# Performance work log

Measured on AMD Instinct MI355X. Metric: run time of the kernel, lower is better.

The kernel has to match this reference:

```python
import jax, jax.numpy as jnp
import numpy as np


def setup_inputs() -> dict:
    key = jax.random.key(0)
    ks = jax.random.split(key, 5)
    b, n, d = 1, 768, 128
    scale = 1.0 / np.sqrt(d)
    x = jax.random.normal(ks[0], (b, n, d), dtype=jnp.float32)
    W_in = jax.random.normal(ks[1], (d, d), dtype=jnp.float32) * scale
    b_in = jax.random.normal(ks[2], (d,), dtype=jnp.float32) * 0.02
    W_out = jax.random.normal(ks[3], (d, d), dtype=jnp.float32) * scale
    b_out = jax.random.normal(ks[4], (d,), dtype=jnp.float32) * 0.02
    return {"x": x, "W_in": W_in, "b_in": b_in, "W_out": W_out, "b_out": b_out}


def reference(x, W_in, b_in, W_out, b_out):
    # proj_in applied to x (original calls it twice on the same input; identical result)
    left = jnp.einsum('bid,ed->bie', x, W_in) + b_in          # [b, n, d]
    # broadcast outer product: [b, i, 1, d] * [b, 1, j, d] -> [b, i, j, d]
    outer = left[:, :, None, :] * left[:, None, :, :]
    # proj_out over feature dim
    out = jnp.einsum('bijd,ed->bije', outer, W_out) + b_out    # [b, n, n, d]
    return out
```

## Files before the change

### kernel.cpp

```cpp
#include <hip/hip_runtime.h>

#define Nn 768
#define Dd 128
#define LDP 136

typedef __attribute__((ext_vector_type(8))) short bf16x8;
typedef __attribute__((ext_vector_type(4))) float f32x4;
typedef __attribute__((ext_vector_type(4))) int   i32x4;

static __device__ __forceinline__ unsigned short f2bf(float f) {
  unsigned int u = __builtin_bit_cast(unsigned int, f);
  u += 0x7fffu + ((u >> 16) & 1u);
  return (unsigned short)(u >> 16);
}
static __device__ __forceinline__ float bf2f(unsigned short h) {
  unsigned int u = ((unsigned int)h) << 16;
  return __builtin_bit_cast(float, u);
}
static __device__ __forceinline__ unsigned int cvtpk(float lo, float hi) {
  unsigned int r;
  asm("v_cvt_pk_bf16_f32 %0, %1, %2" : "=v"(r) : "v"(lo), "v"(hi));
  return r;
}

__global__ __launch_bounds__(128)
void k_left(const float* __restrict__ x, const float* __restrict__ Win,
            const float* __restrict__ bin, unsigned short* __restrict__ left) {
  __shared__ float sx[Dd];
  const int i = blockIdx.x;
  const int e = threadIdx.x;
  sx[e] = x[i * Dd + e];
  __syncthreads();
  const float4* wrow = (const float4*)(Win + e * Dd);
  float a0 = 0.f, a1 = 0.f, a2 = 0.f, a3 = 0.f;
#pragma unroll
  for (int d4 = 0; d4 < Dd / 4; d4 += 4) {
    float4 w0 = wrow[d4+0], w1 = wrow[d4+1], w2 = wrow[d4+2], w3 = wrow[d4+3];
    a0 += sx[4*d4+ 0]*w0.x + sx[4*d4+ 1]*w0.y + sx[4*d4+ 2]*w0.z + sx[4*d4+ 3]*w0.w;
    a1 += sx[4*d4+ 4]*w1.x + sx[4*d4+ 5]*w1.y + sx[4*d4+ 6]*w1.z + sx[4*d4+ 7]*w1.w;
    a2 += sx[4*d4+ 8]*w2.x + sx[4*d4+ 9]*w2.y + sx[4*d4+10]*w2.z + sx[4*d4+11]*w2.w;
    a3 += sx[4*d4+12]*w3.x + sx[4*d4+13]*w3.y + sx[4*d4+14]*w3.z + sx[4*d4+15]*w3.w;
  }
  left[i * Dd + e] = f2bf(((a0 + a1) + (a2 + a3)) + bin[e]);
}

__global__ __launch_bounds__(256, 4)
void k_outer(const unsigned short* __restrict__ left, const float* __restrict__ Wout,
             const float* __restrict__ bout, float* __restrict__ out) {
  __shared__ __attribute__((aligned(16))) unsigned short sB[128 * LDP];
  __shared__ float sLi[Dd];
  __shared__ float sBo[Dd];

  const int jt = blockIdx.x;
  const int i  = blockIdx.y;
  const int t  = threadIdx.x;

  if (t < Dd) {
    sLi[t] = bf2f(left[i * Dd + t]);
    sBo[t] = bout[t];
  }
  __syncthreads();

  {
    const int row = t >> 4;
    const int c8  = (t & 15) * 8;
    float l[8];
#pragma unroll
    for (int q = 0; q < 8; ++q) l[q] = sLi[c8 + q];
#pragma unroll
    for (int it = 0; it < 8; ++it) {
      const int r = row + it * 16;
      const float4* wp = (const float4*)(Wout + r * Dd + c8);
      float4 w0 = wp[0], w1 = wp[1];
      i32x4 vb;
      vb[0] = (int)cvtpk(w0.x * l[0], w0.y * l[1]);
      vb[1] = (int)cvtpk(w0.z * l[2], w0.w * l[3]);
      vb[2] = (int)cvtpk(w1.x * l[4], w1.y * l[5]);
      vb[3] = (int)cvtpk(w1.z * l[6], w1.w * l[7]);
      *(i32x4*)(sB + r * LDP + c8) = vb;
    }
  }
  __syncthreads();

  const int wid  = t >> 6;
  const int lane = t & 63;
  const int l15  = lane & 15;
  const int kq   = (lane >> 4) * 8;

  float bias[8];
#pragma unroll
  for (int n = 0; n < 8; ++n) bias[n] = sBo[n * 16 + l15];

  const unsigned short* gA = left + (size_t)(jt * 128 + wid * 32 + l15) * Dd;
  bf16x8 A0[4], A1[4];
#pragma unroll
  for (int kb = 0; kb < 4; ++kb) {
    A0[kb] = *(const bf16x8*)(gA + kb * 32 + kq);
    A1[kb] = *(const bf16x8*)(gA + 16 * Dd + kb * 32 + kq);
  }

  f32x4 acc[2][8] = {};
#pragma unroll
  for (int n = 0; n < 8; ++n) {
    const unsigned short* sBrow = sB + (n * 16 + l15) * LDP + kq;
#pragma unroll
    for (int kb = 0; kb < 4; ++kb) {
      bf16x8 b = *(const bf16x8*)(sBrow + kb * 32);
      acc[0][n] = __builtin_amdgcn_mfma_f32_16x16x32_bf16(A0[kb], b, acc[0][n], 0, 0, 0);
      acc[1][n] = __builtin_amdgcn_mfma_f32_16x16x32_bf16(A1[kb], b, acc[1][n], 0, 0, 0);
    }
  }

#pragma unroll
  for (int jb = 0; jb < 2; ++jb) {
#pragma unroll
    for (int r = 0; r < 4; ++r) {
      const int j = jt * 128 + wid * 32 + jb * 16 + (lane >> 4) * 4 + r;
      float* orow = out + ((size_t)i * Nn + j) * Dd;
#pragma unroll
      for (int n = 0; n < 8; ++n) {
        orow[n * 16 + l15] = acc[jb][n][r] + bias[n];
      }
    }
  }
}

extern "C" void kernel_launch(void* const* d_in, const int* in_sizes, int n_in,
                              void* d_out, int out_size, void* d_ws, size_t ws_size,
                              hipStream_t stream) {
  const float* x    = (const float*)d_in[0];
  const float* Win  = (const float*)d_in[1];
  const float* bin  = (const float*)d_in[2];
  const float* Wout = (const float*)d_in[3];
  const float* bout = (const float*)d_in[4];
  float* out = (float*)d_out;
  unsigned short* left = (unsigned short*)d_ws;

  k_left<<<Nn, Dd, 0, stream>>>(x, Win, bin, left);
  dim3 grid(Nn / 128, Nn);
  k_outer<<<grid, 256, 0, stream>>>(left, Wout, bout, out);
}
```

Baseline: 62.33 us.

## Precompute per-row scaled Wout in workspace and drop in-kernel LDS staging

A new prep kernel computes the left projection and, for every row i, the bf16 matrix Wout scaled by left[i], writing all of them (about 25 MB) to workspace. The main outer kernel then streams A and B straight from global memory into MFMA with no LDS staging and no barriers. This removes the sixfold redundant B construction per i, since six j-tiles previously each rebuilt it. In exchange it adds a large global write and read of B_all, which competes with the output write bandwidth. The old two-kernel path is kept as a fallback when the workspace is too small.

```diff
diff --git a/kernel.cpp b/kernel.cpp
--- a/kernel.cpp
+++ b/kernel.cpp
@@ -21,6 +21,101 @@
   unsigned int r;
   asm("v_cvt_pk_bf16_f32 %0, %1, %2" : "=v"(r) : "v"(lo), "v"(hi));
   return r;
+}
+
+__global__ __launch_bounds__(256)
+void k_prep(const float* __restrict__ x, const float* __restrict__ Win,
+            const float* __restrict__ bin, const float* __restrict__ Wout,
+            unsigned short* __restrict__ left, unsigned short* __restrict__ B_all) {
+  __shared__ float sx[Dd];
+  __shared__ float sL[Dd];
+  const int i = blockIdx.x;
+  const int t = threadIdx.x;
+
+  if (t < Dd) sx[t] = x[i * Dd + t];
+  __syncthreads();
+
+  if (t < Dd) {
+    const float4* wrow = (const float4*)(Win + t * Dd);
+    float a0 = 0.f, a1 = 0.f, a2 = 0.f, a3 = 0.f;
+#pragma unroll
+    for (int d4 = 0; d4 < Dd / 4; d4 += 4) {
+      float4 w0 = wrow[d4+0], w1 = wrow[d4+1], w2 = wrow[d4+2], w3 = wrow[d4+3];
+      a0 += sx[4*d4+ 0]*w0.x + sx[4*d4+ 1]*w0.y + sx[4*d4+ 2]*w0.z + sx[4*d4+ 3]*w0.w;
+      a1 += sx[4*d4+ 4]*w1.x + sx[4*d4+ 5]*w1.y + sx[4*d4+ 6]*w1.z + sx[4*d4+ 7]*w1.w;
+      a2 += sx[4*d4+ 8]*w2.x + sx[4*d4+ 9]*w2.y + sx[4*d4+10]*w2.z + sx[4*d4+11]*w2.w;
+      a3 += sx[4*d4+12]*w3.x + sx[4*d4+13]*w3.y + sx[4*d4+14]*w3.z + sx[4*d4+15]*w3.w;
+    }
+    const float v = ((a0 + a1) + (a2 + a3)) + bin[t];
+    sL[t] = v;
+    left[i * Dd + t] = f2bf(v);
+  }
+  __syncthreads();
+
+  {
+    const int r  = t >> 1;
+    const int c0 = (t & 1) * 64;
+    const float4* wp = (const float4*)(Wout + r * Dd + c0);
+    unsigned short* brow = B_all + (size_t)i * (Dd * Dd) + r * Dd + c0;
+    const float* lp = sL + c0;
+#pragma unroll
+    for (int q = 0; q < 8; ++q) {
+      float4 w0 = wp[2*q], w1 = wp[2*q+1];
+      i32x4 vb;
+      vb[0] = (int)cvtpk(w0.x * lp[8*q+0], w0.y * lp[8*q+1]);
+      vb[1] = (int)cvtpk(w0.z * lp[8*q+2], w0.w * lp[8*q+3]);
+      vb[2] = (int)cvtpk(w1.x * lp[8*q+4], w1.y * lp[8*q+5]);
+      vb[3] = (int)cvtpk(w1.z * lp[8*q+6], w1.w * lp[8*q+7]);
+      *(i32x4*)(brow + q * 8) = vb;
+    }
+  }
+}
+
+__global__ __launch_bounds__(256, 4)
+void k_outer_pure(const unsigned short* __restrict__ left,
+                  const unsigned short* __restrict__ B_all,
+                  const float* __restrict__ bout, float* __restrict__ out) {
+  const int jt = blockIdx.x;
+  const int i  = blockIdx.y;
+  const int t  = threadIdx.x;
+
+  const int wid  = t >> 6;
+  const int lane = t & 63;
+  const int l15  = lane & 15;
+  const int koct = (lane >> 4) * 8;
+
+  float bias[8];
+#pragma unroll
+  for (int n = 0; n < 8; ++n) bias[n] = bout[n * 16 + l15];
+
+  const unsigned short* gA = left + (size_t)(jt * 128 + wid * 32 + l15) * Dd + koct;
+  const unsigned short* gB = B_all + (size_t)i * (Dd * Dd) + l15 * Dd + koct;
+
+  f32x4 acc[2][8] = {};
+#pragma unroll
+  for (int kb = 0; kb < 4; ++kb) {
+    bf16x8 a0 = *(const bf16x8*)(gA + kb * 32);
+    bf16x8 a1 = *(const bf16x8*)(gA + 16 * Dd + kb * 32);
+#pragma unroll
+    for (int n = 0; n < 8; ++n) {
+      bf16x8 b = *(const bf16x8*)(gB + n * 16 * Dd + kb * 32);
+      acc[0][n] = __builtin_amdgcn_mfma_f32_16x16x32_bf16(a0, b, acc[0][n], 0, 0, 0);
+      acc[1][n] = __builtin_amdgcn_mfma_f32_16x16x32_bf16(a1, b, acc[1][n], 0, 0, 0);
+    }
+  }
+
+#pragma unroll
+  for (int jb = 0; jb < 2; ++jb) {
+#pragma unroll
+    for (int r = 0; r < 4; ++r) {
+      const int j = jt * 128 + wid * 32 + jb * 16 + (lane >> 4) * 4 + r;
+      float* orow = out + ((size_t)i * Nn + j) * Dd;
+#pragma unroll
+      for (int n = 0; n < 8; ++n) {
+        orow[n * 16 + l15] = acc[jb][n][r] + bias[n];
+      }
+    }
+  }
 }
 
 __global__ __launch_bounds__(128)
@@ -45,8 +140,8 @@
 }
 
 __global__ __launch_bounds__(256, 4)
-void k_outer(const unsigned short* __restrict__ left, const float* __restrict__ Wout,
-             const float* __restrict__ bout, float* __restrict__ out) {
+void k_outer_r9(const unsigned short* __restrict__ left, const float* __restrict__ Wout,
+                const float* __restrict__ bout, float* __restrict__ out) {
   __shared__ __attribute__((aligned(16))) unsigned short sB[128 * LDP];
   __shared__ float sLi[Dd];
   __shared__ float sBo[Dd];
@@ -55,12 +150,8 @@
   const int i  = blockIdx.y;
   const int t  = threadIdx.x;
 
-  if (t < Dd) {
-    sLi[t] = bf2f(left[i * Dd + t]);
-    sBo[t] = bout[t];
-  }
-  __syncthreads();
-
+  if (t < Dd) { sLi[t] = bf2f(left[i * Dd + t]); sBo[t] = bout[t]; }
+  __syncthreads();
   {
     const int row = t >> 4;
     const int c8  = (t & 15) * 8;
@@ -110,7 +201,6 @@
       acc[1][n] = __builtin_amdgcn_mfma_f32_16x16x32_bf16(A1[kb], b, acc[1][n], 0, 0, 0);
     }
   }
-
 #pragma unroll
   for (int jb = 0; jb < 2; ++jb) {
 #pragma unroll
@@ -134,9 +224,17 @@
   const float* Wout = (const float*)d_in[3];
   const float* bout = (const float*)d_in[4];
   float* out = (float*)d_out;
-  unsigned short* left = (unsigned short*)d_ws;
-
-  k_left<<<Nn, Dd, 0, stream>>>(x, Win, bin, left);
+
+  const size_t NEED = 262144 + (size_t)Nn * Dd * Dd * 2;
   dim3 grid(Nn / 128, Nn);
-  k_outer<<<grid, 256, 0, stream>>>(left, Wout, bout, out);
-}
+  if (ws_size >= NEED) {
+    unsigned short* left  = (unsigned short*)d_ws;
+    unsigned short* B_all = (unsigned short*)((char*)d_ws + 262144);
+    k_prep<<<Nn, 256, 0, stream>>>(x, Win, bin, Wout, left, B_all);
+    k_outer_pure<<<grid, 256, 0, stream>>>(left, B_all, bout, out);
+  } else {
+    unsigned short* left = (unsigned short*)d_ws;
+    k_left<<<Nn, Dd, 0, stream>>>(x, Win, bin, left);
+    k_outer_r9<<<grid, 256, 0, stream>>>(left, Wout, bout, out);
+  }
+}
```

Measured after the change: 143.4 us. 2.3x slower.

## Precompute bf16 W_out once and fold left_i scaling into A operand

Applied to the files above, without the earlier changes.

W_out is now converted to bf16 once, by extra blocks appended to the first kernel. The per-row scaling by left_i moves from the shared-memory B tile to the A fragments held in registers, using fp32 left_i values from a new workspace buffer. This removes the per-block fp32 W_out load, multiply and convert, plus one of the two barriers in the outer-product kernel, so the B tile becomes a plain bf16 copy. In exchange, each block now does register-side multiply and convert work on the A operand and reads extra workspace buffers.

```diff
diff --git a/kernel.cpp b/kernel.cpp
--- a/kernel.cpp
+++ b/kernel.cpp
@@ -13,19 +13,36 @@
   u += 0x7fffu + ((u >> 16) & 1u);
   return (unsigned short)(u >> 16);
 }
-static __device__ __forceinline__ float bf2f(unsigned short h) {
-  unsigned int u = ((unsigned int)h) << 16;
-  return __builtin_bit_cast(float, u);
-}
 static __device__ __forceinline__ unsigned int cvtpk(float lo, float hi) {
   unsigned int r;
   asm("v_cvt_pk_bf16_f32 %0, %1, %2" : "=v"(r) : "v"(lo), "v"(hi));
   return r;
 }
+static __device__ __forceinline__ float bfhi(unsigned int u) {
+  return __builtin_bit_cast(float, u & 0xffff0000u);
+}
+static __device__ __forceinline__ float bflo(unsigned int u) {
+  return __builtin_bit_cast(float, u << 16);
+}
 
 __global__ __launch_bounds__(128)
 void k_left(const float* __restrict__ x, const float* __restrict__ Win,
-            const float* __restrict__ bin, unsigned short* __restrict__ left) {
+            const float* __restrict__ bin, const float* __restrict__ Wout,
+            unsigned short* __restrict__ left, float* __restrict__ left_f,
+            unsigned short* __restrict__ wout_bf) {
+  if (blockIdx.x >= Nn) {
+    const int idx = (blockIdx.x - Nn) * 128 + threadIdx.x;
+    const float4* src = (const float4*)(Wout + idx * 16);
+    float4 w0 = src[0], w1 = src[1], w2 = src[2], w3 = src[3];
+    i32x4 o0, o1;
+    o0[0] = (int)cvtpk(w0.x, w0.y); o0[1] = (int)cvtpk(w0.z, w0.w);
+    o0[2] = (int)cvtpk(w1.x, w1.y); o0[3] = (int)cvtpk(w1.z, w1.w);
+    o1[0] = (int)cvtpk(w2.x, w2.y); o1[1] = (int)cvtpk(w2.z, w2.w);
+    o1[2] = (int)cvtpk(w3.x, w3.y); o1[3] = (int)cvtpk(w3.z, w3.w);
+    *(i32x4*)(wout_bf + idx * 16)     = o0;
+    *(i32x4*)(wout_bf + idx * 16 + 8) = o1;
+    return;
+  }
   __shared__ float sx[Dd];
   const int i = blockIdx.x;
   const int e = threadIdx.x;
@@ -41,46 +58,29 @@
     a2 += sx[4*d4+ 8]*w2.x + sx[4*d4+ 9]*w2.y + sx[4*d4+10]*w2.z + sx[4*d4+11]*w2.w;
     a3 += sx[4*d4+12]*w3.x + sx[4*d4+13]*w3.y + sx[4*d4+14]*w3.z + sx[4*d4+15]*w3.w;
   }
-  left[i * Dd + e] = f2bf(((a0 + a1) + (a2 + a3)) + bin[e]);
+  const float v = ((a0 + a1) + (a2 + a3)) + bin[e];
+  left_f[i * Dd + e] = v;
+  left[i * Dd + e]   = f2bf(v);
 }
 
 __global__ __launch_bounds__(256, 4)
-void k_outer(const unsigned short* __restrict__ left, const float* __restrict__ Wout,
+void k_outer(const unsigned short* __restrict__ left,
+             const float* __restrict__ left_f,
+             const unsigned short* __restrict__ wout_bf,
              const float* __restrict__ bout, float* __restrict__ out) {
   __shared__ __attribute__((aligned(16))) unsigned short sB[128 * LDP];
-  __shared__ float sLi[Dd];
-  __shared__ float sBo[Dd];
 
   const int jt = blockIdx.x;
   const int i  = blockIdx.y;
   const int t  = threadIdx.x;
 
-  if (t < Dd) {
-    sLi[t] = bf2f(left[i * Dd + t]);
-    sBo[t] = bout[t];
+#pragma unroll
+  for (int it = 0; it < 8; ++it) {
+    const int idx16 = t + it * 256;
+    const int r  = idx16 >> 4;
+    const int c8 = (idx16 & 15) * 8;
+    *(i32x4*)(sB + r * LDP + c8) = *(const i32x4*)(wout_bf + r * Dd + c8);
   }
-  __syncthreads();
-
-  {
-    const int row = t >> 4;
-    const int c8  = (t & 15) * 8;
-    float l[8];
-#pragma unroll
-    for (int q = 0; q < 8; ++q) l[q] = sLi[c8 + q];
-#pragma unroll
-    for (int it = 0; it < 8; ++it) {
-      const int r = row + it * 16;
-      const float4* wp = (const float4*)(Wout + r * Dd + c8);
-      float4 w0 = wp[0], w1 = wp[1];
-      i32x4 vb;
-      vb[0] = (int)cvtpk(w0.x * l[0], w0.y * l[1]);
-      vb[1] = (int)cvtpk(w0.z * l[2], w0.w * l[3]);
-      vb[2] = (int)cvtpk(w1.x * l[4], w1.y * l[5]);
-      vb[3] = (int)cvtpk(w1.z * l[6], w1.w * l[7]);
-      *(i32x4*)(sB + r * LDP + c8) = vb;
-    }
-  }
-  __syncthreads();
 
   const int wid  = t >> 6;
   const int lane = t & 63;
@@ -89,15 +89,35 @@
 
   float bias[8];
 #pragma unroll
-  for (int n = 0; n < 8; ++n) bias[n] = sBo[n * 16 + l15];
+  for (int n = 0; n < 8; ++n) bias[n] = bout[n * 16 + l15];
 
-  const unsigned short* gA = left + (size_t)(jt * 128 + wid * 32 + l15) * Dd;
-  bf16x8 A0[4], A1[4];
+  float lif[4][8];
 #pragma unroll
   for (int kb = 0; kb < 4; ++kb) {
-    A0[kb] = *(const bf16x8*)(gA + kb * 32 + kq);
-    A1[kb] = *(const bf16x8*)(gA + 16 * Dd + kb * 32 + kq);
+    const float4* lp = (const float4*)(left_f + i * Dd + kb * 32 + kq);
+    float4 f0 = lp[0], f1 = lp[1];
+    lif[kb][0]=f0.x; lif[kb][1]=f0.y; lif[kb][2]=f0.z; lif[kb][3]=f0.w;
+    lif[kb][4]=f1.x; lif[kb][5]=f1.y; lif[kb][6]=f1.z; lif[kb][7]=f1.w;
   }
+
+  bf16x8 Ap[2][4];
+#pragma unroll
+  for (int jb = 0; jb < 2; ++jb) {
+    const unsigned short* gL = left + (size_t)(jt * 128 + wid * 32 + jb * 16 + l15) * Dd + kq;
+#pragma unroll
+    for (int kb = 0; kb < 4; ++kb) {
+      i32x4 a = *(const i32x4*)(gL + kb * 32);
+      i32x4 vb;
+#pragma unroll
+      for (int w = 0; w < 4; ++w) {
+        const unsigned int u = (unsigned int)a[w];
+        vb[w] = (int)cvtpk(bflo(u) * lif[kb][2*w], bfhi(u) * lif[kb][2*w+1]);
+      }
+      Ap[jb][kb] = __builtin_bit_cast(bf16x8, vb);
+    }
+  }
+
+  __syncthreads();
 
   f32x4 acc[2][8] = {};
 #pragma unroll
@@ -106,8 +126,8 @@
 #pragma unroll
     for (int kb = 0; kb < 4; ++kb) {
       bf16x8 b = *(const bf16x8*)(sBrow + kb * 32);
-      acc[0][n] = __builtin_amdgcn_mfma_f32_16x16x32_bf16(A0[kb], b, acc[0][n], 0, 0, 0);
-      acc[1][n] = __builtin_amdgcn_mfma_f32_16x16x32_bf16(A1[kb], b, acc[1][n], 0, 0, 0);
+      acc[0][n] = __builtin_amdgcn_mfma_f32_16x16x32_bf16(Ap[0][kb], b, acc[0][n], 0, 0, 0);
+      acc[1][n] = __builtin_amdgcn_mfma_f32_16x16x32_bf16(Ap[1][kb], b, acc[1][n], 0, 0, 0);
     }
   }
 
@@ -134,9 +154,12 @@
   const float* Wout = (const float*)d_in[3];
   const float* bout = (const float*)d_in[4];
   float* out = (float*)d_out;
-  unsigned short* left = (unsigned short*)d_ws;
 
-  k_left<<<Nn, Dd, 0, stream>>>(x, Win, bin, left);
+  unsigned short* left    = (unsigned short*)d_ws;
+  float*          left_f  = (float*)((char*)d_ws + 256 * 1024);
+  unsigned short* wout_bf = (unsigned short*)((char*)d_ws + 768 * 1024);
+
+  k_left<<<Nn + 8, Dd, 0, stream>>>(x, Win, bin, Wout, left, left_f, wout_bf);
   dim3 grid(Nn / 128, Nn);
-  k_outer<<<grid, 256, 0, stream>>>(left, Wout, bout, out);
+  k_outer<<<grid, 256, 0, stream>>>(left, left_f, wout_bf, bout, out);
 }
```

Result: no change. 62.30 us, median of 2 (-0.0%).
